# Performance work log

Measured on AMD Instinct MI355X. Metric: run time of the kernel, lower is better.

The kernel has to match this reference:

```python
import jax, jax.numpy as jnp
import numpy as np

B = 8192; L = 50; D_EMB = 128
N_USER = 100000; N_MOVIE = 50000; N_DENSE = 8
D = 2 * D_EMB + D_EMB + N_DENSE  # 392 total_input_dim
E = 4; T = 2; H1 = 256; H2 = 128; ATT_H = 64; N_CROSS = 3


def setup_inputs() -> dict:
    key = jax.random.key(0)
    ks = jax.random.split(key, 28)
    rn = lambda k, shape, s=0.02: jax.random.normal(k, shape, jnp.float32) * s
    inp = {
        'userId': jax.random.randint(ks[0], (B,), 0, N_USER),
        'movieId': jax.random.randint(ks[1], (B,), 0, N_MOVIE),
        'seq_history': jax.random.randint(ks[2], (B, L), 0, N_MOVIE),
        'dense_feats': jax.random.normal(ks[3], (B, N_DENSE), jnp.float32),
        # embeddings (row 0 is padding_idx -> zeros)
        'emb_user': rn(ks[4], (N_USER + 1, D_EMB)).at[0].set(0.0),
        'emb_movie': rn(ks[5], (N_MOVIE + 1, D_EMB)).at[0].set(0.0),
        # DIN attention MLP: input [q,k,q-k,q*k] = 4*D_EMB
        'att_w1': rn(ks[6], (4 * D_EMB, ATT_H)), 'att_b1': jnp.zeros((ATT_H,), jnp.float32),
        'att_w2': rn(ks[7], (ATT_H, 1)), 'att_b2': jnp.zeros((1,), jnp.float32),
        # LayerNorms
        'in_gamma': jnp.ones((D,), jnp.float32), 'in_beta': jnp.zeros((D,), jnp.float32),
        'cr_gamma': jnp.ones((D,), jnp.float32), 'cr_beta': jnp.zeros((D,), jnp.float32),
        # CrossNetV2: x_{l+1} = x0 * (x_l W_l + b_l) + x_l
        'cross_W': rn(ks[8], (N_CROSS, D, D)), 'cross_b': jnp.zeros((N_CROSS, D), jnp.float32),
        # MMoE experts: Linear(D,H1)-ReLU-Linear(H1,H2), batched over E
        'exp_w1': rn(ks[9], (E, D, H1)), 'exp_b1': jnp.zeros((E, H1), jnp.float32),
        'exp_w2': rn(ks[10], (E, H1, H2)), 'exp_b2': jnp.zeros((E, H2), jnp.float32),
        # gates per task
        'gate_w': rn(ks[11], (T, D, E)), 'gate_b': jnp.zeros((T, E), jnp.float32),
        # task heads Linear(H2, 1)
        'head_w': rn(ks[12], (T, H2)), 'head_b': jnp.zeros((T,), jnp.float32),
    }
    return inp


def _layernorm(x, g, b, eps=1e-5):
    m = jnp.mean(x, axis=-1, keepdims=True)
    v = jnp.var(x, axis=-1, keepdims=True)
    return (x - m) * jax.lax.rsqrt(v + eps) * g + b


def _forward(userId, movieId, seq_history, dense_feats, emb_user, emb_movie,
             att_w1, att_b1, att_w2, att_b2, in_gamma, in_beta,
             cross_W, cross_b, cr_gamma, cr_beta,
             exp_w1, exp_b1, exp_w2, exp_b2, gate_w, gate_b, head_w, head_b):
    # sparse embedding gathers
    user_e = emb_user[userId]            # [B, D_EMB]
    movie_e = emb_movie[movieId]         # [B, D_EMB]  (target item)
    hist = emb_movie[seq_history]        # [B, L, D_EMB]
    mask = seq_history > 0               # [B, L]

    # DIN attention pooling
    q = jnp.broadcast_to(movie_e[:, None, :], hist.shape)            # [B, L, D_EMB]
    att_in = jnp.concatenate([q, hist, q - hist, q * hist], axis=-1)  # [B, L, 4*D_EMB]
    scores = (jax.nn.relu(att_in @ att_w1 + att_b1) @ att_w2 + att_b2)[..., 0]  # [B, L]
    scores = jnp.where(mask, scores, -1e9)
    probs = jax.nn.softmax(scores, axis=-1)                           # [B, L]
    interest = jnp.einsum('bl,bld->bd', probs, hist)                  # [B, D_EMB]

    x = jnp.concatenate([user_e, movie_e, interest, dense_feats], axis=-1)  # [B, D]
    x = _layernorm(x, in_gamma, in_beta)

    # CrossNetV2
    x0 = x
    for l in range(N_CROSS):
        x = x0 * (x @ cross_W[l] + cross_b[l]) + x
    x = _layernorm(x, cr_gamma, cr_beta)

    # MMoE: batched expert GEMMs + per-task soft gates
    h = jax.nn.relu(jnp.einsum('bd,edh->ebh', x, exp_w1) + exp_b1[:, None, :])  # [E,B,H1]
    eo = jnp.einsum('ebh,eho->ebo', h, exp_w2) + exp_b2[:, None, :]             # [E,B,H2]
    g = jax.nn.softmax(jnp.einsum('bd,tde->tbe', x, gate_w) + gate_b[:, None, :], axis=-1)  # [T,B,E]
    task_feat = jnp.einsum('tbe,ebo->tbo', g, eo)                                # [T,B,H2]

    logits = jnp.einsum('tbo,to->tb', task_feat, head_w) + head_b[:, None]       # [T,B]
    return logits


def reference(userId, movieId, seq_history, dense_feats, emb_user, emb_movie,
              att_w1, att_b1, att_w2, att_b2, in_gamma, in_beta,
              cross_W, cross_b, cr_gamma, cr_beta,
              exp_w1, exp_b1, exp_w2, exp_b2, gate_w, gate_b, head_w, head_b):
    return _forward(userId, movieId, seq_history, dense_feats, emb_user, emb_movie,
                    att_w1, att_b1, att_w2, att_b2, in_gamma, in_beta,
                    cross_W, cross_b, cr_gamma, cr_beta,
                    exp_w1, exp_b1, exp_w2, exp_b2, gate_w, gate_b, head_w, head_b)
```

## Files before the change

### kernel.cpp

```cpp
#include <hip/hip_runtime.h>
#include <hip/hip_bf16.h>

typedef short short8 __attribute__((ext_vector_type(8)));
typedef short short4v __attribute__((ext_vector_type(4)));
typedef float f32x4 __attribute__((ext_vector_type(4)));

constexpr int BB = 8192;
constexpr int LL = 50;
constexpr int DE = 128;
constexpr int DD = 392;
constexpr int HH1 = 256;
constexpr int HH2 = 128;

__device__ __forceinline__ short f2b(float x) {
    __hip_bfloat16 h = __float2bfloat16(x);
    return __builtin_bit_cast(short, h);
}
__device__ __forceinline__ float b2f(short v) {
    unsigned u = ((unsigned)(unsigned short)v) << 16;
    return __builtin_bit_cast(float, u);
}

__global__ __launch_bounds__(256) void prep_small(
    const float* __restrict__ w1,
    const float* __restrict__ w2, const float* __restrict__ b2,
    const float* __restrict__ head_w,
    short* __restrict__ WqpT, float* __restrict__ WkpFf,
    float* __restrict__ hw2, float* __restrict__ hc)
{
    __shared__ float hw[256];
    const int b = blockIdx.x, t = threadIdx.x;
    if (b < 32) {
        int o = b * 256 + t;
        int h = o >> 7, d = o & 127;
        WqpT[o] = f2b(w1[d * 64 + h] + w1[16384 + d * 64 + h]);
    } else if (b < 64) {
        int o = (b - 32) * 256 + t;
        int e = o & 7, lane = (o >> 3) & 63, nt = (o >> 9) & 3, kt = o >> 11;
        int k = (kt << 5) + ((lane >> 4) << 3) + e;
        int h = (nt << 4) + (lane & 15);
        int base = (o >> 3) << 4;
        WkpFf[base + e]     = w1[(128 + k) * 64 + h] - w1[(256 + k) * 64 + h];
        WkpFf[base + 8 + e] = w1[(384 + k) * 64 + h];
    } else {
        const int e = b - 64;
        hw[t] = head_w[t];
        __syncthreads();
        const float* row = &w2[((long)e * HH1 + t) * HH2];
        float s0 = 0.f, s1 = 0.f;
        #pragma unroll 8
        for (int o = 0; o < 128; o += 4) {
            float4 v = *reinterpret_cast<const float4*>(&row[o]);
            s0 += v.x * hw[o] + v.y * hw[o + 1] + v.z * hw[o + 2] + v.w * hw[o + 3];
            s1 += v.x * hw[128 + o] + v.y * hw[129 + o] + v.z * hw[130 + o] + v.w * hw[131 + o];
        }
        hw2[(((e << 8) + t) << 1) + 0] = s0;
        hw2[(((e << 8) + t) << 1) + 1] = s1;
        if (t < 2) {
            float s = 0.f;
            for (int o = 0; o < 128; ++o) s += b2[e * 128 + o] * hw[t * 128 + o];
            hc[e * 2 + t] = s;
        }
    }
}

constexpr int S0 = 3 * 392 * 392;
constexpr int S1 = 4 * 392 * 256;
constexpr int S2 = (50001 * 128) / 4;
constexpr int S3 = (BB * 128) / 4;

__global__ __launch_bounds__(256) void prep_trans(
    const float* __restrict__ cross_W, const float* __restrict__ exp_w1,
    const float* __restrict__ emb_movie, const int* __restrict__ movieId,
    short* __restrict__ WTc, short* __restrict__ WT1, short* __restrict__ embB,
    short* __restrict__ qb)
{
    int idx = blockIdx.x * 256 + threadIdx.x;
    if (idx < S0) {
        int z = idx / (392 * 392), rr = idx - z * 392 * 392;
        int c = rr / 392, r = rr - c * 392;
        WTc[idx] = f2b(cross_W[(long)z * 153664 + r * 392 + c]);
    } else if (idx < S0 + S1) {
        int j = idx - S0;
        int z = j / 100352, rr = j - z * 100352;
        int c = rr / 392, r = rr - c * 392;
        WT1[j] = f2b(exp_w1[(long)z * 100352 + r * 256 + c]);
    } else if (idx < S0 + S1 + S2) {
        long j = (long)(idx - S0 - S1) << 2;
        float4 v = *reinterpret_cast<const float4*>(&emb_movie[j]);
        short4v o;
        o[0] = f2b(v.x); o[1] = f2b(v.y); o[2] = f2b(v.z); o[3] = f2b(v.w);
        *reinterpret_cast<short4v*>(&embB[j]) = o;
    } else if (idx < S0 + S1 + S2 + S3) {
        int j = idx - S0 - S1 - S2;
        int bb = j >> 5, d0 = (j & 31) << 2;
        float4 v = *reinterpret_cast<const float4*>(
            &emb_movie[(long)movieId[bb] * DE + d0]);
        short4v o;
        o[0] = f2b(v.x); o[1] = f2b(v.y); o[2] = f2b(v.z); o[3] = f2b(v.w);
        *reinterpret_cast<short4v*>(&qb[bb * DE + d0]) = o;
    }
}

__global__ __launch_bounds__(256, 8) void attn_kernel(
    const int* __restrict__ userId, const int* __restrict__ movieId,
    const int* __restrict__ seq, const float* __restrict__ dense,
    const float* __restrict__ emb_user, const float* __restrict__ emb_movie,
    const short* __restrict__ embB,
    const float* __restrict__ qcAll, const float* __restrict__ WkpFf,
    const float* __restrict__ att_w2, const float* __restrict__ att_b2,
    const float* __restrict__ in_gamma, const float* __restrict__ in_beta,
    float* __restrict__ x0f, short* __restrict__ x0b)
{
    __shared__ short hist[64 * 128];
    __shared__ float qs[128];
    __shared__ int   seq_s[64];
    __shared__ float spS[4][64];
    __shared__ float probs[64];
    __shared__ float ibuf[4][128];
    __shared__ float stats[2];

    const int b = blockIdx.x;
    const int t = threadIdx.x;
    const int lane = t & 63;
    const int w = t >> 6;

    if (t < 128) qs[t] = emb_movie[(long)movieId[b] * DE + t];
    if (t < 64)  seq_s[t] = (t < LL) ? seq[b * LL + t] : 0;
    __syncthreads();

    #pragma unroll
    for (int i = 0; i < 4; ++i) {
        const int idx = t + (i << 8);
        const int l = idx >> 4, c = idx & 15;
        short8 hv = *reinterpret_cast<const short8*>(&embB[(long)seq_s[l] * DE + (c << 3)]);
        const int byte = (l << 8) + ((c << 4) ^ ((l & 7) << 4));
        *reinterpret_cast<short8*>(reinterpret_cast<char*>(hist) + byte) = hv;
    }

    const int col = (w << 4) + (lane & 15);
    float ue = (t < 128) ? emb_user[(long)userId[b] * DE + t] : 0.f;
    float dv = (t >= 128 && t < 136) ? dense[b * 8 + (t - 128)] : 0.f;
    const float qc  = qcAll[((long)b << 6) + col];
    const float w2v = att_w2[col];

    short8 bfrag[4];
    #pragma unroll
    for (int kt = 0; kt < 4; ++kt) {
        const float* wkp = &WkpFf[((((kt << 2) + w) << 6) | lane) << 4];
        const int kq = (kt << 5) + ((lane >> 4) << 3);
        #pragma unroll
        for (int j = 0; j < 8; ++j)
            bfrag[kt][j] = f2b(fmaf(qs[kq + j], wkp[8 + j], wkp[j]));
    }
    __syncthreads();

    #pragma unroll
    for (int mt = 0; mt < 4; ++mt) {
        f32x4 acc = {0.f, 0.f, 0.f, 0.f};
        const int row = (mt << 4) + (lane & 15);
        const int rbase = row << 8;
        const int swz = (row & 7) << 4;
        #pragma unroll
        for (int kt = 0; kt < 4; ++kt) {
            const int kbyte = (kt << 6) + ((lane >> 4) << 4);
            short8 a = *reinterpret_cast<const short8*>(
                reinterpret_cast<char*>(hist) + rbase + (kbyte ^ swz));
            acc = __builtin_amdgcn_mfma_f32_16x16x32_bf16(a, bfrag[kt], acc, 0, 0, 0);
        }
        #pragma unroll
        for (int r = 0; r < 4; ++r) {
            float v = fmaxf(acc[r] + qc, 0.f) * w2v;
            v += __shfl_xor(v, 1); v += __shfl_xor(v, 2);
            v += __shfl_xor(v, 4); v += __shfl_xor(v, 8);
            if ((lane & 15) == 0)
                spS[w][(mt << 4) + ((lane >> 4) << 2) + r] = v;
        }
    }
    __syncthreads();

    if (t < 64) {
        float sc = spS[0][t] + spS[1][t] + spS[2][t] + spS[3][t] + att_b2[0];
        float s = (t < LL) ? ((seq_s[t] > 0) ? sc : -1e9f) : -INFINITY;
        float m = s;
        #pragma unroll
        for (int off = 32; off > 0; off >>= 1) m = fmaxf(m, __shfl_xor(m, off));
        float e = (t < LL) ? __expf(s - m) : 0.f;
        float sum = e;
        #pragma unroll
        for (int off = 32; off > 0; off >>= 1) sum += __shfl_xor(sum, off);
        probs[t] = (t < LL) ? (e / sum) : 0.f;
    }
    __syncthreads();

    const int g  = t >> 5;
    const int d0 = (t & 31) << 2;
    float4 ps = make_float4(0.f, 0.f, 0.f, 0.f);
    #pragma unroll
    for (int i = 0; i < 8; ++i) {
        const int l = g + (i << 3);
        const int byte = (l << 8) + ((d0 << 1) ^ ((l & 7) << 4));
        short4v hv = *reinterpret_cast<const short4v*>(
            reinterpret_cast<const char*>(hist) + byte);
        const float p = probs[l];
        ps.x = fmaf(p, b2f(hv[0]), ps.x);
        ps.y = fmaf(p, b2f(hv[1]), ps.y);
        ps.z = fmaf(p, b2f(hv[2]), ps.z);
        ps.w = fmaf(p, b2f(hv[3]), ps.w);
    }
    ps.x += __shfl_xor(ps.x, 32); ps.y += __shfl_xor(ps.y, 32);
    ps.z += __shfl_xor(ps.z, 32); ps.w += __shfl_xor(ps.w, 32);
    if (lane < 32)
        *reinterpret_cast<float4*>(&ibuf[w][lane << 2]) = ps;
    __syncthreads();

    float v0 = (t < 128) ? ue : qs[t - 128];
    float v1 = 0.f;
    if (t < 128)       v1 = ibuf[0][t] + ibuf[1][t] + ibuf[2][t] + ibuf[3][t];
    else if (t < 136)  v1 = dv;

    float s2 = v0 + v1, q2 = v0 * v0 + v1 * v1;
    #pragma unroll
    for (int off = 32; off > 0; off >>= 1) {
        s2 += __shfl_xor(s2, off);
        q2 += __shfl_xor(q2, off);
    }
    if (lane == 0) { spS[0][w] = s2; spS[1][w] = q2; }
    __syncthreads();
    if (t == 0) {
        float S = spS[0][0] + spS[0][1] + spS[0][2] + spS[0][3];
        float Q = spS[1][0] + spS[1][1] + spS[1][2] + spS[1][3];
        float mean = S / (float)DD;
        float var = Q / (float)DD - mean * mean;
        stats[0] = mean;
        stats[1] = rsqrtf(var + 1e-5f);
    }
    __syncthreads();
    const float mean = stats[0], inv = stats[1];
    const long base = (long)b * DD;
    float o0 = (v0 - mean) * inv * in_gamma[t] + in_beta[t];
    x0f[base + t] = o0; x0b[base + t] = f2b(o0);
    if (t < 136) {
        float o1 = (v1 - mean) * inv * in_gamma[256 + t] + in_beta[256 + t];
        x0f[base + 256 + t] = o1; x0b[base + 256 + t] = f2b(o1);
    }
}

template<int MODE, int WF32, int WB16, int NXB, int NZB>
__global__ __launch_bounds__(256) void bgemm(
    const short* __restrict__ A, const short* __restrict__ WT,
    const float* __restrict__ bias,
    float* __restrict__ outF, short* __restrict__ outB,
    const float* __restrict__ x0, const float* __restrict__ xin,
    int M, int N, int K, long aZ, long wZ, long bZ, long oZ)
{
    __shared__ short As[2][64 * 64];
    __shared__ short Bs[2][64 * 64];

    int id = blockIdx.x;
    const int qq = (int)gridDim.x >> 3;
    id = (id & 7) * qq + (id >> 3);
    const int mb  = id / (NXB * NZB);
    const int rem = id - mb * (NXB * NZB);
    const int z   = rem / NXB;
    const int xb  = rem - z * NXB;

    A += (long)z * aZ; WT += (long)z * wZ; bias += (long)z * bZ;
    const long oz = (long)z * oZ;

    const int t = threadIdx.x, w = t >> 6, lane = t & 63;
    const int m0 = mb * 64, n0 = xb * 64;
    const int sm = t >> 3, sk8 = (t & 7) << 3;

    f32x4 acc[4];
    #pragma unroll
    for (int i = 0; i < 4; ++i) {
        #pragma unroll
        for (int r = 0; r < 4; ++r) acc[i][r] = 0.f;
    }

    const int nsteps = (K + 63) >> 6;
    short8 avA[2], bvA[2], avB[2], bvB[2];

    auto loadA = [&](int k0) {
        #pragma unroll
        for (int i = 0; i < 2; ++i) {
            const int r = sm + (i << 5);
            short8 zv = {0, 0, 0, 0, 0, 0, 0, 0};
            avA[i] = zv; bvA[i] = zv;
            if (k0 + sk8 < K) {
                avA[i] = *reinterpret_cast<const short8*>(&A[(long)(m0 + r) * K + k0 + sk8]);
                if (n0 + r < N)
                    bvA[i] = *reinterpret_cast<const short8*>(&WT[(long)(n0 + r) * K + k0 + sk8]);
            }
        }
    };
    auto loadB = [&](int k0) {
        #pragma unroll
        for (int i = 0; i < 2; ++i) {
            const int r = sm + (i << 5);
            short8 zv = {0, 0, 0, 0, 0, 0, 0, 0};
            avB[i] = zv; bvB[i] = zv;
            if (k0 + sk8 < K) {
                avB[i] = *reinterpret_cast<const short8*>(&A[(long)(m0 + r) * K + k0 + sk8]);
                if (n0 + r < N)
                    bvB[i] = *reinterpret_cast<const short8*>(&WT[(long)(n0 + r) * K + k0 + sk8]);
            }
        }
    };
    auto wrA = [&](int buf) {
        #pragma unroll
        for (int i = 0; i < 2; ++i) {
            const int r = sm + (i << 5);
            const int byte = (r << 7) + ((sk8 << 1) ^ ((r & 7) << 4));
            *reinterpret_cast<short8*>(reinterpret_cast<char*>(&As[buf][0]) + byte) = avA[i];
            *reinterpret_cast<short8*>(reinterpret_cast<char*>(&Bs[buf][0]) + byte) = bvA[i];
        }
    };
    auto wrB = [&](int buf) {
        #pragma unroll
        for (int i = 0; i < 2; ++i) {
            const int r = sm + (i << 5);
            const int byte = (r << 7) + ((sk8 << 1) ^ ((r & 7) << 4));
            *reinterpret_cast<short8*>(reinterpret_cast<char*>(&As[buf][0]) + byte) = avB[i];
            *reinterpret_cast<short8*>(reinterpret_cast<char*>(&Bs[buf][0]) + byte) = bvB[i];
        }
    };
    auto domfma = [&](int buf) {
        #pragma unroll
        for (int kt = 0; kt < 2; ++kt) {
            const int kbyte = (kt << 6) + ((lane >> 4) << 4);
            const int ar = (w << 4) + (lane & 15);
            short8 a = *reinterpret_cast<const short8*>(
                reinterpret_cast<char*>(&As[buf][0]) + (ar << 7) + (kbyte ^ ((ar & 7) << 4)));
            #pragma unroll
            for (int nt = 0; nt < 4; ++nt) {
                const int br = (nt << 4) + (lane & 15);
                short8 bb = *reinterpret_cast<const short8*>(
                    reinterpret_cast<char*>(&Bs[buf][0]) + (br << 7) + (kbyte ^ ((br & 7) << 4)));
                acc[nt] = __builtin_amdgcn_mfma_f32_16x16x32_bf16(a, bb, acc[nt], 0, 0, 0);
            }
        }
    };

    loadA(0);
    wrA(0);
    if (nsteps > 1) loadA(64);
    if (nsteps > 2) loadB(128);
    __syncthreads();

    int cur = 0, s = 0;
    while (s + 1 < nsteps) {
        domfma(cur);
        wrA(cur ^ 1);
        if (s + 3 < nsteps) loadA((s + 3) << 6);
        __syncthreads(); cur ^= 1; ++s;
        if (s + 1 < nsteps) {
            domfma(cur);
            wrB(cur ^ 1);
            if (s + 3 < nsteps) loadB((s + 3) << 6);
            __syncthreads(); cur ^= 1; ++s;
        }
    }
    domfma(cur);

    #pragma unroll
    for (int nt = 0; nt < 4; ++nt) {
        const int col = n0 + (nt << 4) + (lane & 15);
        if (col < N) {
            const float bv = bias[col];
            #pragma unroll
            for (int r = 0; r < 4; ++r) {
                const int row = m0 + (w << 4) + ((lane >> 4) << 2) + r;
                float v = acc[nt][r] + bv;
                if (MODE == 1) v = fmaxf(v, 0.f);
                const long o = (long)row * N + col;
                if (MODE == 2) v = x0[o] * v + xin[o];
                if (WF32) outF[oz + o] = v;
                if (WB16) outB[oz + o] = f2b(v);
            }
        }
    }
}

__global__ __launch_bounds__(256) void ln_kernel(
    const float* __restrict__ in,
    const float* __restrict__ gamma, const float* __restrict__ beta,
    float* __restrict__ outF, short* __restrict__ outB)
{
    __shared__ float red[2][4];
    __shared__ float stats[2];
    const int b = blockIdx.x, t = threadIdx.x, lane = t & 63, w = t >> 6;
    const long base = (long)b * DD;
    float v0 = in[base + t];
    float v1 = (t < 136) ? in[base + 256 + t] : 0.f;
    float s = v0 + v1, q2 = v0 * v0 + v1 * v1;
    #pragma unroll
    for (int off = 32; off > 0; off >>= 1) {
        s += __shfl_xor(s, off);
        q2 += __shfl_xor(q2, off);
    }
    if (lane == 0) { red[0][w] = s; red[1][w] = q2; }
    __syncthreads();
    if (t == 0) {
        float S = red[0][0] + red[0][1] + red[0][2] + red[0][3];
        float Q = red[1][0] + red[1][1] + red[1][2] + red[1][3];
        float mean = S / (float)DD;
        float var = Q / (float)DD - mean * mean;
        stats[0] = mean;
        stats[1] = rsqrtf(var + 1e-5f);
    }
    __syncthreads();
    const float mean = stats[0], inv = stats[1];
    float o0 = (v0 - mean) * inv * gamma[t] + beta[t];
    outF[base + t] = o0; outB[base + t] = f2b(o0);
    if (t < 136) {
        float o1 = (v1 - mean) * inv * gamma[256 + t] + beta[256 + t];
        outF[base + 256 + t] = o1; outB[base + 256 + t] = f2b(o1);
    }
}

__global__ __launch_bounds__(256) void final_kernel(
    const float* __restrict__ x, const short* __restrict__ h1,
    const float* __restrict__ hw2, const float* __restrict__ hc,
    const float* __restrict__ gate_w, const float* __restrict__ gate_b,
    const float* __restrict__ head_b, float* __restrict__ out)
{
    const int t = threadIdx.x, lane = t & 63, w = t >> 6;
    const int b = blockIdx.x * 4 + w;
    const float* xr = x + (long)b * DD;

    float xv[7];
    #pragma unroll
    for (int i = 0; i < 7; ++i) {
        int d = lane + (i << 6);
        xv[i] = (d < DD) ? xr[d] : 0.f;
    }

    float gl[8] = {0.f, 0.f, 0.f, 0.f, 0.f, 0.f, 0.f, 0.f};
    #pragma unroll
    for (int i = 0; i < 7; ++i) {
        int d = lane + (i << 6);
        if (d < DD) {
            float4 g0 = *reinterpret_cast<const float4*>(&gate_w[d << 2]);
            float4 g1 = *reinterpret_cast<const float4*>(&gate_w[1568 + (d << 2)]);
            gl[0] = fmaf(xv[i], g0.x, gl[0]); gl[1] = fmaf(xv[i], g0.y, gl[1]);
            gl[2] = fmaf(xv[i], g0.z, gl[2]); gl[3] = fmaf(xv[i], g0.w, gl[3]);
            gl[4] = fmaf(xv[i], g1.x, gl[4]); gl[5] = fmaf(xv[i], g1.y, gl[5]);
            gl[6] = fmaf(xv[i], g1.z, gl[6]); gl[7] = fmaf(xv[i], g1.w, gl[7]);
        }
    }

    float ed[8];
    #pragma unroll
    for (int e = 0; e < 4; ++e) {
        short4v hv = *reinterpret_cast<const short4v*>(
            &h1[((long)e * BB + b) * HH1 + (lane << 2)]);
        const float* hwp = &hw2[(((e << 8) + (lane << 2))) << 1];
        float4 w01 = *reinterpret_cast<const float4*>(hwp);
        float4 w23 = *reinterpret_cast<const float4*>(hwp + 4);
        float h0 = b2f(hv[0]), h1f = b2f(hv[1]), h2 = b2f(hv[2]), h3 = b2f(hv[3]);
        ed[e]     = fmaf(h0, w01.x, fmaf(h1f, w01.z, fmaf(h2, w23.x, h3 * w23.z)));
        ed[4 + e] = fmaf(h0, w01.y, fmaf(h1f, w01.w, fmaf(h2, w23.y, h3 * w23.w)));
    }

    #pragma unroll
    for (int v = 0; v < 8; ++v) {
        #pragma unroll
        for (int off = 32; off > 0; off >>= 1) {
            gl[v] += __shfl_xor(gl[v], off);
            ed[v] += __shfl_xor(ed[v], off);
        }
    }

    if (lane == 0) {
        float res[2];
        #pragma unroll
        for (int tt = 0; tt < 2; ++tt) {
            float lv[4], m = -1e30f;
            #pragma unroll
            for (int e = 0; e < 4; ++e) {
                lv[e] = gl[tt * 4 + e] + gate_b[tt * 4 + e];
                m = fmaxf(m, lv[e]);
            }
            float sum = 0.f, acc = 0.f;
            #pragma unroll
            for (int e = 0; e < 4; ++e) { lv[e] = __expf(lv[e] - m); sum += lv[e]; }
            #pragma unroll
            for (int e = 0; e < 4; ++e)
                acc = fmaf(lv[e], ed[tt * 4 + e] + hc[e * 2 + tt], acc);
            res[tt] = head_b[tt] + acc / sum;
        }
        out[b] = res[0];
        out[BB + b] = res[1];
    }
}

extern "C" void kernel_launch(void* const* d_in, const int* in_sizes, int n_in,
                              void* d_out, int out_size, void* d_ws, size_t ws_size,
                              hipStream_t stream) {
    const int*   userId    = (const int*)d_in[0];
    const int*   movieId   = (const int*)d_in[1];
    const int*   seq       = (const int*)d_in[2];
    const float* dense     = (const float*)d_in[3];
    const float* emb_user  = (const float*)d_in[4];
    const float* emb_movie = (const float*)d_in[5];
    const float* att_w1    = (const float*)d_in[6];
    const float* att_b1    = (const float*)d_in[7];
    const float* att_w2    = (const float*)d_in[8];
    const float* att_b2    = (const float*)d_in[9];
    const float* in_gamma  = (const float*)d_in[10];
    const float* in_beta   = (const float*)d_in[11];
    const float* cr_gamma  = (const float*)d_in[12];
    const float* cr_beta   = (const float*)d_in[13];
    const float* cross_W   = (const float*)d_in[14];
    const float* cross_b   = (const float*)d_in[15];
    const float* exp_w1    = (const float*)d_in[16];
    const float* exp_b1    = (const float*)d_in[17];
    const float* exp_w2    = (const float*)d_in[18];
    const float* exp_b2    = (const float*)d_in[19];
    const float* gate_w    = (const float*)d_in[20];
    const float* gate_b    = (const float*)d_in[21];
    const float* head_w    = (const float*)d_in[22];
    const float* head_b    = (const float*)d_in[23];
    float* outp = (float*)d_out;

    char* p = (char*)d_ws;
    auto alloc = [&](size_t bytes) -> char* {
        char* r = p; p += (bytes + 255) & ~(size_t)255; return r;
    };
    short* WqpT  = (short*)alloc(8192 * 2);
    float* WkpFf = (float*)alloc(16384 * 4);
    float* hw2 = (float*)alloc(2048 * 4);
    float* hc  = (float*)alloc(8 * 4);
    short* WTc = (short*)alloc((size_t)3 * 392 * 392 * 2);
    short* WT1 = (short*)alloc((size_t)4 * 256 * 392 * 2);
    short* embB = (short*)alloc((size_t)50001 * 128 * 2);
    short* qb   = (short*)alloc((size_t)BB * DE * 2);
    float* qcAll = (float*)alloc((size_t)BB * 64 * 4);
    float* x0f = (float*)alloc((size_t)BB * DD * 4);
    short* x0b = (short*)alloc((size_t)BB * DD * 2);
    float* xAf = (float*)alloc((size_t)BB * DD * 4);
    short* xAb = (short*)alloc((size_t)BB * DD * 2);
    float* xBf = (float*)alloc((size_t)BB * DD * 4);
    short* xBb = (short*)alloc((size_t)BB * DD * 2);
    short* h1b = (short*)alloc((size_t)4 * BB * HH1 * 2);

    prep_small<<<68, 256, 0, stream>>>(att_w1, exp_w2, exp_b2, head_w,
                                       WqpT, WkpFf, hw2, hc);
    prep_trans<<<(S0 + S1 + S2 + S3 + 255) / 256, 256, 0, stream>>>(
        cross_W, exp_w1, emb_movie, movieId, WTc, WT1, embB, qb);

    bgemm<0, 1, 0, 1, 1><<<128, 256, 0, stream>>>(
        qb, WqpT, att_b1, qcAll, nullptr, nullptr, nullptr,
        BB, 64, DE, 0, 0, 0, 0);

    attn_kernel<<<BB, 256, 0, stream>>>(userId, movieId, seq, dense,
                                        emb_user, emb_movie, embB,
                                        qcAll, WkpFf,
                                        att_w2, att_b2,
                                        in_gamma, in_beta, x0f, x0b);

    bgemm<2, 1, 1, 7, 1><<<896, 256, 0, stream>>>(x0b, WTc, cross_b, xAf, xAb,
                                                  x0f, x0f, BB, DD, DD, 0, 0, 0, 0);
    bgemm<2, 1, 1, 7, 1><<<896, 256, 0, stream>>>(xAb, WTc + 392 * 392, cross_b + 392,
                                                  xBf, xBb, x0f, xAf, BB, DD, DD, 0, 0, 0, 0);
    bgemm<2, 1, 0, 7, 1><<<896, 256, 0, stream>>>(xBb, WTc + 2 * 392 * 392, cross_b + 784,
                                                  xAf, nullptr, x0f, xBf, BB, DD, DD, 0, 0, 0, 0);

    ln_kernel<<<BB, 256, 0, stream>>>(xAf, cr_gamma, cr_beta, xBf, xBb);

    bgemm<1, 0, 1, 4, 4><<<2048, 256, 0, stream>>>(
        xBb, WT1, exp_b1, nullptr, h1b, nullptr, nullptr,
        BB, HH1, DD, 0, (long)HH1 * DD, HH1, (long)BB * HH1);

    final_kernel<<<BB / 4, 256, 0, stream>>>(xBf, h1b, hw2, hc,
                                             gate_w, gate_b, head_b, outp);

    (void)in_sizes; (void)n_in; (void)out_size; (void)ws_size;
}
```

Measured before the change: 177.2 us.

## Merge prep kernels, compute query projection in prep, two samples per attention block

```diff
diff --git a/kernel.cpp b/kernel.cpp
--- a/kernel.cpp
+++ b/kernel.cpp
@@ -21,29 +21,37 @@
     return __builtin_bit_cast(float, u);
 }
 
-__global__ __launch_bounds__(256) void prep_small(
+constexpr int S0 = 3 * 392 * 392;
+constexpr int S1 = 4 * 392 * 256;
+constexpr int S2 = (50001 * 128) / 4;
+constexpr int NB_TRANS = 9619;
+constexpr int QC0 = 36 + NB_TRANS;
+constexpr int NB_PREP = QC0 + 2048;
+
+__global__ __launch_bounds__(256) void prep_all(
     const float* __restrict__ w1,
     const float* __restrict__ w2, const float* __restrict__ b2,
-    const float* __restrict__ head_w,
-    short* __restrict__ WqpT, float* __restrict__ WkpFf,
-    float* __restrict__ hw2, float* __restrict__ hc)
+    const float* __restrict__ head_w, const float* __restrict__ att_b1,
+    const float* __restrict__ cross_W, const float* __restrict__ exp_w1,
+    const float* __restrict__ emb_movie, const int* __restrict__ movieId,
+    short* __restrict__ WkpFb, float* __restrict__ hw2, float* __restrict__ hc,
+    short* __restrict__ WTc, short* __restrict__ WT1, short* __restrict__ embB,
+    float* __restrict__ qcAll)
 {
-    __shared__ float hw[256];
-    const int b = blockIdx.x, t = threadIdx.x;
-    if (b < 32) {
-        int o = b * 256 + t;
-        int h = o >> 7, d = o & 127;
-        WqpT[o] = f2b(w1[d * 64 + h] + w1[16384 + d * 64 + h]);
-    } else if (b < 64) {
-        int o = (b - 32) * 256 + t;
+    __shared__ float sh[4][128];
+    const int blk = blockIdx.x, t = threadIdx.x;
+
+    if (blk < 32) {
+        int o = blk * 256 + t;
         int e = o & 7, lane = (o >> 3) & 63, nt = (o >> 9) & 3, kt = o >> 11;
         int k = (kt << 5) + ((lane >> 4) << 3) + e;
         int h = (nt << 4) + (lane & 15);
         int base = (o >> 3) << 4;
-        WkpFf[base + e]     = w1[(128 + k) * 64 + h] - w1[(256 + k) * 64 + h];
-        WkpFf[base + 8 + e] = w1[(384 + k) * 64 + h];
-    } else {
-        const int e = b - 64;
+        WkpFb[base + e]     = f2b(w1[(128 + k) * 64 + h] - w1[(256 + k) * 64 + h]);
+        WkpFb[base + 8 + e] = f2b(w1[(384 + k) * 64 + h]);
+    } else if (blk < 36) {
+        const int e = blk - 32;
+        float* hw = &sh[0][0];
         hw[t] = head_w[t];
         __syncthreads();
         const float* row = &w2[((long)e * HH1 + t) * HH2];
@@ -61,188 +69,220 @@
             for (int o = 0; o < 128; ++o) s += b2[e * 128 + o] * hw[t * 128 + o];
             hc[e * 2 + t] = s;
         }
-    }
-}
-
-constexpr int S0 = 3 * 392 * 392;
-constexpr int S1 = 4 * 392 * 256;
-constexpr int S2 = (50001 * 128) / 4;
-constexpr int S3 = (BB * 128) / 4;
-
-__global__ __launch_bounds__(256) void prep_trans(
-    const float* __restrict__ cross_W, const float* __restrict__ exp_w1,
-    const float* __restrict__ emb_movie, const int* __restrict__ movieId,
-    short* __restrict__ WTc, short* __restrict__ WT1, short* __restrict__ embB,
-    short* __restrict__ qb)
-{
-    int idx = blockIdx.x * 256 + threadIdx.x;
-    if (idx < S0) {
-        int z = idx / (392 * 392), rr = idx - z * 392 * 392;
-        int c = rr / 392, r = rr - c * 392;
-        WTc[idx] = f2b(cross_W[(long)z * 153664 + r * 392 + c]);
-    } else if (idx < S0 + S1) {
-        int j = idx - S0;
-        int z = j / 100352, rr = j - z * 100352;
-        int c = rr / 392, r = rr - c * 392;
-        WT1[j] = f2b(exp_w1[(long)z * 100352 + r * 256 + c]);
-    } else if (idx < S0 + S1 + S2) {
-        long j = (long)(idx - S0 - S1) << 2;
-        float4 v = *reinterpret_cast<const float4*>(&emb_movie[j]);
-        short4v o;
-        o[0] = f2b(v.x); o[1] = f2b(v.y); o[2] = f2b(v.z); o[3] = f2b(v.w);
-        *reinterpret_cast<short4v*>(&embB[j]) = o;
-    } else if (idx < S0 + S1 + S2 + S3) {
-        int j = idx - S0 - S1 - S2;
-        int bb = j >> 5, d0 = (j & 31) << 2;
-        float4 v = *reinterpret_cast<const float4*>(
-            &emb_movie[(long)movieId[bb] * DE + d0]);
-        short4v o;
-        o[0] = f2b(v.x); o[1] = f2b(v.y); o[2] = f2b(v.z); o[3] = f2b(v.w);
-        *reinterpret_cast<short4v*>(&qb[bb * DE + d0]) = o;
-    }
-}
-
-__global__ __launch_bounds__(256, 8) void attn_kernel(
+    } else if (blk < QC0) {
+        int idx = (blk - 36) * 256 + t;
+        if (idx < S0) {
+            int z = idx / (392 * 392), rr = idx - z * 392 * 392;
+            int c = rr / 392, r = rr - c * 392;
+            WTc[idx] = f2b(cross_W[(long)z * 153664 + r * 392 + c]);
+        } else if (idx < S0 + S1) {
+            int j = idx - S0;
+            int z = j / 100352, rr = j - z * 100352;
+            int c = rr / 392, r = rr - c * 392;
+            WT1[j] = f2b(exp_w1[(long)z * 100352 + r * 256 + c]);
+        } else if (idx < S0 + S1 + S2) {
+            long j = (long)(idx - S0 - S1) << 2;
+            float4 v = *reinterpret_cast<const float4*>(&emb_movie[j]);
+            short4v o;
+            o[0] = f2b(v.x); o[1] = f2b(v.y); o[2] = f2b(v.z); o[3] = f2b(v.w);
+            *reinterpret_cast<short4v*>(&embB[j]) = o;
+        }
+    } else {
+        const int w = t >> 6, lane = t & 63;
+        const int b = (blk - QC0) * 4 + w;
+        if (lane < 32)
+            *reinterpret_cast<float4*>(&sh[w][lane << 2]) =
+                *reinterpret_cast<const float4*>(
+                    &emb_movie[(long)movieId[b] * DE + (lane << 2)]);
+        __syncthreads();
+        float s = att_b1[lane];
+        #pragma unroll 8
+        for (int d = 0; d < 128; ++d)
+            s = fmaf(sh[w][d], w1[d * 64 + lane] + w1[16384 + d * 64 + lane], s);
+        qcAll[((long)b << 6) + lane] = s;
+    }
+}
+
+__global__ __launch_bounds__(256, 4) void attn_kernel(
     const int* __restrict__ userId, const int* __restrict__ movieId,
     const int* __restrict__ seq, const float* __restrict__ dense,
     const float* __restrict__ emb_user, const float* __restrict__ emb_movie,
     const short* __restrict__ embB,
-    const float* __restrict__ qcAll, const float* __restrict__ WkpFf,
+    const float* __restrict__ qcAll, const short* __restrict__ WkpFb,
     const float* __restrict__ att_w2, const float* __restrict__ att_b2,
     const float* __restrict__ in_gamma, const float* __restrict__ in_beta,
     float* __restrict__ x0f, short* __restrict__ x0b)
 {
-    __shared__ short hist[64 * 128];
-    __shared__ float qs[128];
-    __shared__ int   seq_s[64];
-    __shared__ float spS[4][64];
-    __shared__ float probs[64];
-    __shared__ float ibuf[4][128];
-    __shared__ float stats[2];
-
-    const int b = blockIdx.x;
-    const int t = threadIdx.x;
-    const int lane = t & 63;
-    const int w = t >> 6;
-
-    if (t < 128) qs[t] = emb_movie[(long)movieId[b] * DE + t];
-    if (t < 64)  seq_s[t] = (t < LL) ? seq[b * LL + t] : 0;
-    __syncthreads();
-
+    __shared__ __align__(16) char lds[35360];
+    float* qsA   = reinterpret_cast<float*>(lds + 26624);
+    float* spS   = reinterpret_cast<float*>(lds + 27648);
+    float* probs = reinterpret_cast<float*>(lds + 29696);
+    float* ibuf  = reinterpret_cast<float*>(lds + 30208);
+    float* ubuf  = reinterpret_cast<float*>(lds + 34304);
+    float* stats = reinterpret_cast<float*>(lds + 35328);
+
+    const int t = threadIdx.x, lane = t & 63, w = t >> 6;
+    const int b0 = blockIdx.x << 1, b1 = b0 + 1;
+
+    if (t < 32)
+        *reinterpret_cast<float4*>(&qsA[t << 2]) =
+            *reinterpret_cast<const float4*>(&emb_movie[(long)movieId[b0] * DE + (t << 2)]);
+    else if (t < 64)
+        *reinterpret_cast<float4*>(&qsA[128 + ((t - 32) << 2)]) =
+            *reinterpret_cast<const float4*>(&emb_movie[(long)movieId[b1] * DE + ((t - 32) << 2)]);
+
+    if (t < 128) ubuf[t] = emb_user[(long)userId[b0] * DE + t];
+    else         ubuf[t] = emb_user[(long)userId[b1] * DE + (t - 128)];
+
+    float dv0 = 0.f, dv1 = 0.f;
+    if (t >= 128 && t < 136) {
+        dv0 = dense[b0 * 8 + t - 128];
+        dv1 = dense[b1 * 8 + t - 128];
+    }
+    int ms = 0;
+    if (w < 2 && lane < LL) ms = seq[(w ? b1 : b0) * LL + lane];
+
+    const int col = (w << 4) + (lane & 15);
+    const float qcv[2] = { qcAll[((long)b0 << 6) + col], qcAll[((long)b1 << 6) + col] };
+    const float w2v = att_w2[col];
+
+    const int g0 = t >> 4, c = t & 15;
     #pragma unroll
     for (int i = 0; i < 4; ++i) {
-        const int idx = t + (i << 8);
-        const int l = idx >> 4, c = idx & 15;
-        short8 hv = *reinterpret_cast<const short8*>(&embB[(long)seq_s[l] * DE + (c << 3)]);
-        const int byte = (l << 8) + ((c << 4) ^ ((l & 7) << 4));
-        *reinterpret_cast<short8*>(reinterpret_cast<char*>(hist) + byte) = hv;
-    }
-
-    const int col = (w << 4) + (lane & 15);
-    float ue = (t < 128) ? emb_user[(long)userId[b] * DE + t] : 0.f;
-    float dv = (t >= 128 && t < 136) ? dense[b * 8 + (t - 128)] : 0.f;
-    const float qc  = qcAll[((long)b << 6) + col];
-    const float w2v = att_w2[col];
-
-    short8 bfrag[4];
-    #pragma unroll
-    for (int kt = 0; kt < 4; ++kt) {
-        const float* wkp = &WkpFf[((((kt << 2) + w) << 6) | lane) << 4];
-        const int kq = (kt << 5) + ((lane >> 4) << 3);
-        #pragma unroll
-        for (int j = 0; j < 8; ++j)
-            bfrag[kt][j] = f2b(fmaf(qs[kq + j], wkp[8 + j], wkp[j]));
-    }
-    __syncthreads();
-
-    #pragma unroll
-    for (int mt = 0; mt < 4; ++mt) {
-        f32x4 acc = {0.f, 0.f, 0.f, 0.f};
-        const int row = (mt << 4) + (lane & 15);
-        const int rbase = row << 8;
-        const int swz = (row & 7) << 4;
+        const int l = g0 + (i << 4);
+        if (l < 52) {
+            int sv0 = (l < LL) ? seq[b0 * LL + l] : 0;
+            int sv1 = (l < LL) ? seq[b1 * LL + l] : 0;
+            const int byte = (l << 8) + ((c << 4) ^ ((l & 7) << 4));
+            *reinterpret_cast<short8*>(lds + byte) =
+                *reinterpret_cast<const short8*>(&embB[(long)sv0 * DE + (c << 3)]);
+            *reinterpret_cast<short8*>(lds + 13312 + byte) =
+                *reinterpret_cast<const short8*>(&embB[(long)sv1 * DE + (c << 3)]);
+        }
+    }
+    __syncthreads();
+
+    #pragma unroll
+    for (int r = 0; r < 2; ++r) {
+        const char* histr = lds + r * 13312;
+        const float* qsr = &qsA[r << 7];
+        const float qc = qcv[r];
+        short8 bfrag[4];
         #pragma unroll
         for (int kt = 0; kt < 4; ++kt) {
-            const int kbyte = (kt << 6) + ((lane >> 4) << 4);
-            short8 a = *reinterpret_cast<const short8*>(
-                reinterpret_cast<char*>(hist) + rbase + (kbyte ^ swz));
-            acc = __builtin_amdgcn_mfma_f32_16x16x32_bf16(a, bfrag[kt], acc, 0, 0, 0);
-        }
-        #pragma unroll
-        for (int r = 0; r < 4; ++r) {
-            float v = fmaxf(acc[r] + qc, 0.f) * w2v;
-            v += __shfl_xor(v, 1); v += __shfl_xor(v, 2);
-            v += __shfl_xor(v, 4); v += __shfl_xor(v, 8);
-            if ((lane & 15) == 0)
-                spS[w][(mt << 4) + ((lane >> 4) << 2) + r] = v;
-        }
-    }
-    __syncthreads();
-
-    if (t < 64) {
-        float sc = spS[0][t] + spS[1][t] + spS[2][t] + spS[3][t] + att_b2[0];
-        float s = (t < LL) ? ((seq_s[t] > 0) ? sc : -1e9f) : -INFINITY;
+            const int fo = ((((kt << 2) + w) << 6) | lane) << 4;
+            short8 wk = *reinterpret_cast<const short8*>(&WkpFb[fo]);
+            short8 wp = *reinterpret_cast<const short8*>(&WkpFb[fo + 8]);
+            const int kq = (kt << 5) + ((lane >> 4) << 3);
+            #pragma unroll
+            for (int j = 0; j < 8; ++j)
+                bfrag[kt][j] = f2b(fmaf(qsr[kq + j], b2f(wp[j]), b2f(wk[j])));
+        }
+        #pragma unroll
+        for (int mt = 0; mt < 4; ++mt) {
+            f32x4 acc = {0.f, 0.f, 0.f, 0.f};
+            const int row = (mt << 4) + (lane & 15);
+            const int rbase = row << 8;
+            const int swz = (row & 7) << 4;
+            #pragma unroll
+            for (int kt = 0; kt < 4; ++kt) {
+                const int kbyte = (kt << 6) + ((lane >> 4) << 4);
+                short8 a = *reinterpret_cast<const short8*>(histr + rbase + (kbyte ^ swz));
+                acc = __builtin_amdgcn_mfma_f32_16x16x32_bf16(a, bfrag[kt], acc, 0, 0, 0);
+            }
+            #pragma unroll
+            for (int r4 = 0; r4 < 4; ++r4) {
+                float v = fmaxf(acc[r4] + qc, 0.f) * w2v;
+                v += __shfl_xor(v, 1); v += __shfl_xor(v, 2);
+                v += __shfl_xor(v, 4); v += __shfl_xor(v, 8);
+                if ((lane & 15) == 0)
+                    spS[(r << 8) + (w << 6) + (mt << 4) + ((lane >> 4) << 2) + r4] = v;
+            }
+        }
+    }
+    __syncthreads();
+
+    if (w < 2) {
+        const int r = w;
+        const float* sp = &spS[r << 8];
+        float sc = sp[lane] + sp[64 + lane] + sp[128 + lane] + sp[192 + lane] + att_b2[0];
+        float s = (lane < LL) ? ((ms > 0) ? sc : -1e9f) : -INFINITY;
         float m = s;
         #pragma unroll
         for (int off = 32; off > 0; off >>= 1) m = fmaxf(m, __shfl_xor(m, off));
-        float e = (t < LL) ? __expf(s - m) : 0.f;
+        float e = (lane < LL) ? __expf(s - m) : 0.f;
         float sum = e;
         #pragma unroll
         for (int off = 32; off > 0; off >>= 1) sum += __shfl_xor(sum, off);
-        probs[t] = (t < LL) ? (e / sum) : 0.f;
-    }
-    __syncthreads();
-
-    const int g  = t >> 5;
-    const int d0 = (t & 31) << 2;
-    float4 ps = make_float4(0.f, 0.f, 0.f, 0.f);
-    #pragma unroll
-    for (int i = 0; i < 8; ++i) {
-        const int l = g + (i << 3);
-        const int byte = (l << 8) + ((d0 << 1) ^ ((l & 7) << 4));
-        short4v hv = *reinterpret_cast<const short4v*>(
-            reinterpret_cast<const char*>(hist) + byte);
-        const float p = probs[l];
-        ps.x = fmaf(p, b2f(hv[0]), ps.x);
-        ps.y = fmaf(p, b2f(hv[1]), ps.y);
-        ps.z = fmaf(p, b2f(hv[2]), ps.z);
-        ps.w = fmaf(p, b2f(hv[3]), ps.w);
-    }
-    ps.x += __shfl_xor(ps.x, 32); ps.y += __shfl_xor(ps.y, 32);
-    ps.z += __shfl_xor(ps.z, 32); ps.w += __shfl_xor(ps.w, 32);
-    if (lane < 32)
-        *reinterpret_cast<float4*>(&ibuf[w][lane << 2]) = ps;
-    __syncthreads();
-
-    float v0 = (t < 128) ? ue : qs[t - 128];
-    float v1 = 0.f;
-    if (t < 128)       v1 = ibuf[0][t] + ibuf[1][t] + ibuf[2][t] + ibuf[3][t];
-    else if (t < 136)  v1 = dv;
-
-    float s2 = v0 + v1, q2 = v0 * v0 + v1 * v1;
-    #pragma unroll
-    for (int off = 32; off > 0; off >>= 1) {
-        s2 += __shfl_xor(s2, off);
-        q2 += __shfl_xor(q2, off);
-    }
-    if (lane == 0) { spS[0][w] = s2; spS[1][w] = q2; }
-    __syncthreads();
-    if (t == 0) {
-        float S = spS[0][0] + spS[0][1] + spS[0][2] + spS[0][3];
-        float Q = spS[1][0] + spS[1][1] + spS[1][2] + spS[1][3];
+        probs[(r << 6) + lane] = (lane < LL) ? (e / sum) : 0.f;
+    }
+    __syncthreads();
+
+    const int g = t >> 5, d0 = (t & 31) << 2;
+    #pragma unroll
+    for (int r = 0; r < 2; ++r) {
+        const char* histr = lds + r * 13312;
+        float4 ps = make_float4(0.f, 0.f, 0.f, 0.f);
+        #pragma unroll
+        for (int i = 0; i < 8; ++i) {
+            const int l = g + (i << 3);
+            if (l < LL) {
+                const int byte = (l << 8) + ((d0 << 1) ^ ((l & 7) << 4));
+                short4v hv = *reinterpret_cast<const short4v*>(histr + byte);
+                const float p = probs[(r << 6) + l];
+                ps.x = fmaf(p, b2f(hv[0]), ps.x);
+                ps.y = fmaf(p, b2f(hv[1]), ps.y);
+                ps.z = fmaf(p, b2f(hv[2]), ps.z);
+                ps.w = fmaf(p, b2f(hv[3]), ps.w);
+            }
+        }
+        ps.x += __shfl_xor(ps.x, 32); ps.y += __shfl_xor(ps.y, 32);
+        ps.z += __shfl_xor(ps.z, 32); ps.w += __shfl_xor(ps.w, 32);
+        if (lane < 32)
+            *reinterpret_cast<float4*>(&ibuf[(r << 9) + (w << 7) + ((lane & 31) << 2)]) = ps;
+    }
+    __syncthreads();
+
+    float v0[2], v1[2];
+    #pragma unroll
+    for (int r = 0; r < 2; ++r) {
+        const float* qsr = &qsA[r << 7];
+        const float* ibr = &ibuf[r << 9];
+        float a = (t < 128) ? ubuf[(r << 7) + t] : qsr[t - 128];
+        float bv = 0.f;
+        if (t < 128)      bv = ibr[t] + ibr[128 + t] + ibr[256 + t] + ibr[384 + t];
+        else if (t < 136) bv = r ? dv1 : dv0;
+        v0[r] = a; v1[r] = bv;
+        float s2 = a + bv, q2 = a * a + bv * bv;
+        #pragma unroll
+        for (int off = 32; off > 0; off >>= 1) {
+            s2 += __shfl_xor(s2, off);
+            q2 += __shfl_xor(q2, off);
+        }
+        if (lane == 0) { spS[(r << 7) + w] = s2; spS[(r << 7) + 64 + w] = q2; }
+    }
+    __syncthreads();
+    if (t < 2) {
+        const int r = t;
+        const float* sp = &spS[r << 7];
+        float S = sp[0] + sp[1] + sp[2] + sp[3];
+        float Q = sp[64] + sp[65] + sp[66] + sp[67];
         float mean = S / (float)DD;
         float var = Q / (float)DD - mean * mean;
-        stats[0] = mean;
-        stats[1] = rsqrtf(var + 1e-5f);
-    }
-    __syncthreads();
-    const float mean = stats[0], inv = stats[1];
-    const long base = (long)b * DD;
-    float o0 = (v0 - mean) * inv * in_gamma[t] + in_beta[t];
-    x0f[base + t] = o0; x0b[base + t] = f2b(o0);
-    if (t < 136) {
-        float o1 = (v1 - mean) * inv * in_gamma[256 + t] + in_beta[256 + t];
-        x0f[base + 256 + t] = o1; x0b[base + 256 + t] = f2b(o1);
+        stats[r * 2] = mean;
+        stats[r * 2 + 1] = rsqrtf(var + 1e-5f);
+    }
+    __syncthreads();
+    #pragma unroll
+    for (int r = 0; r < 2; ++r) {
+        const float mean = stats[r * 2], inv = stats[r * 2 + 1];
+        const long base = (long)(r ? b1 : b0) * DD;
+        float o0 = (v0[r] - mean) * inv * in_gamma[t] + in_beta[t];
+        x0f[base + t] = o0; x0b[base + t] = f2b(o0);
+        if (t < 136) {
+            float o1 = (v1[r] - mean) * inv * in_gamma[256 + t] + in_beta[256 + t];
+            x0f[base + 256 + t] = o1; x0b[base + 256 + t] = f2b(o1);
+        }
     }
 }
 
@@ -280,7 +320,7 @@
     }
 
     const int nsteps = (K + 63) >> 6;
-    short8 avA[2], bvA[2], avB[2], bvB[2];
+    short8 avA[2], bvA[2];
 
     auto loadA = [&](int k0) {
         #pragma unroll
@@ -295,19 +335,6 @@
             }
         }
     };
-    auto loadB = [&](int k0) {
-        #pragma unroll
-        for (int i = 0; i < 2; ++i) {
-            const int r = sm + (i << 5);
-            short8 zv = {0, 0, 0, 0, 0, 0, 0, 0};
-            avB[i] = zv; bvB[i] = zv;
-            if (k0 + sk8 < K) {
-                avB[i] = *reinterpret_cast<const short8*>(&A[(long)(m0 + r) * K + k0 + sk8]);
-                if (n0 + r < N)
-                    bvB[i] = *reinterpret_cast<const short8*>(&WT[(long)(n0 + r) * K + k0 + sk8]);
-            }
-        }
-    };
     auto wrA = [&](int buf) {
         #pragma unroll
         for (int i = 0; i < 2; ++i) {
@@ -317,15 +344,6 @@
             *reinterpret_cast<short8*>(reinterpret_cast<char*>(&Bs[buf][0]) + byte) = bvA[i];
         }
     };
-    auto wrB = [&](int buf) {
-        #pragma unroll
-        for (int i = 0; i < 2; ++i) {
-            const int r = sm + (i << 5);
-            const int byte = (r << 7) + ((sk8 << 1) ^ ((r & 7) << 4));
-            *reinterpret_cast<short8*>(reinterpret_cast<char*>(&As[buf][0]) + byte) = avB[i];
-            *reinterpret_cast<short8*>(reinterpret_cast<char*>(&Bs[buf][0]) + byte) = bvB[i];
-        }
-    };
     auto domfma = [&](int buf) {
         #pragma unroll
         for (int kt = 0; kt < 2; ++kt) {
@@ -346,21 +364,15 @@
     loadA(0);
     wrA(0);
     if (nsteps > 1) loadA(64);
-    if (nsteps > 2) loadB(128);
-    __syncthreads();
-
-    int cur = 0, s = 0;
-    while (s + 1 < nsteps) {
+    __syncthreads();
+
+    int cur = 0;
+    for (int s = 0; s + 1 < nsteps; ++s) {
         domfma(cur);
         wrA(cur ^ 1);
-        if (s + 3 < nsteps) loadA((s + 3) << 6);
-        __syncthreads(); cur ^= 1; ++s;
-        if (s + 1 < nsteps) {
-            domfma(cur);
-            wrB(cur ^ 1);
-            if (s + 3 < nsteps) loadB((s + 3) << 6);
-            __syncthreads(); cur ^= 1; ++s;
-        }
+        if (s + 2 < nsteps) loadA((s + 2) << 6);
+        __syncthreads();
+        cur ^= 1;
     }
     domfma(cur);
 
@@ -529,14 +541,12 @@
     auto alloc = [&](size_t bytes) -> char* {
         char* r = p; p += (bytes + 255) & ~(size_t)255; return r;
     };
-    short* WqpT  = (short*)alloc(8192 * 2);
-    float* WkpFf = (float*)alloc(16384 * 4);
+    short* WkpFb = (short*)alloc(16384 * 2);
     float* hw2 = (float*)alloc(2048 * 4);
     float* hc  = (float*)alloc(8 * 4);
     short* WTc = (short*)alloc((size_t)3 * 392 * 392 * 2);
     short* WT1 = (short*)alloc((size_t)4 * 256 * 392 * 2);
     short* embB = (short*)alloc((size_t)50001 * 128 * 2);
-    short* qb   = (short*)alloc((size_t)BB * DE * 2);
     float* qcAll = (float*)alloc((size_t)BB * 64 * 4);
     float* x0f = (float*)alloc((size_t)BB * DD * 4);
     short* x0b = (short*)alloc((size_t)BB * DD * 2);
@@ -546,20 +556,14 @@
     short* xBb = (short*)alloc((size_t)BB * DD * 2);
     short* h1b = (short*)alloc((size_t)4 * BB * HH1 * 2);
 
-    prep_small<<<68, 256, 0, stream>>>(att_w1, exp_w2, exp_b2, head_w,
-                                       WqpT, WkpFf, hw2, hc);
-    prep_trans<<<(S0 + S1 + S2 + S3 + 255) / 256, 256, 0, stream>>>(
-        cross_W, exp_w1, emb_movie, movieId, WTc, WT1, embB, qb);
-
-    bgemm<0, 1, 0, 1, 1><<<128, 256, 0, stream>>>(
-        qb, WqpT, att_b1, qcAll, nullptr, nullptr, nullptr,
-        BB, 64, DE, 0, 0, 0, 0);
-
-    attn_kernel<<<BB, 256, 0, stream>>>(userId, movieId, seq, dense,
-                                        emb_user, emb_movie, embB,
-                                        qcAll, WkpFf,
-                                        att_w2, att_b2,
-                                        in_gamma, in_beta, x0f, x0b);
+    prep_all<<<NB_PREP, 256, 0, stream>>>(
+        att_w1, exp_w2, exp_b2, head_w, att_b1, cross_W, exp_w1,
+        emb_movie, movieId, WkpFb, hw2, hc, WTc, WT1, embB, qcAll);
+
+    attn_kernel<<<BB / 2, 256, 0, stream>>>(userId, movieId, seq, dense,
+                                            emb_user, emb_movie, embB,
+                                            qcAll, WkpFb, att_w2, att_b2,
+                                            in_gamma, in_beta, x0f, x0b);
 
     bgemm<2, 1, 1, 7, 1><<<896, 256, 0, stream>>>(x0b, WTc, cross_b, xAf, xAb,
                                                   x0f, x0f, BB, DD, DD, 0, 0, 0, 0);
```

Result: slower. 192.5 us (+8.6%).
